# Kernel optimization log

Measured on AMD Instinct MI355X. Metric: run time of the kernel, lower is better.

The kernel has to match this reference:

```python
import jax, jax.numpy as jnp
import numpy as np

B, T = 64, 128
IN, H, L, OUT = 512, 1024, 2, 1


def _gru_scan(seq, Wi, Wh, bi, bh):
    # seq: (S, in_dim); PyTorch GRU cell, gate order r, z, n.
    h0 = jnp.zeros((H,), dtype=seq.dtype)
    def step(h, x):
        gi = x @ Wi.T + bi          # (3H,)
        gh = h @ Wh.T + bh          # (3H,)
        r = jax.nn.sigmoid(gi[:H] + gh[:H])
        z = jax.nn.sigmoid(gi[H:2 * H] + gh[H:2 * H])
        n = jnp.tanh(gi[2 * H:] + r * gh[2 * H:])
        h_new = (1.0 - z) * n + z * h
        return h_new, h_new
    _, hs = jax.lax.scan(step, h0, seq)
    return hs                        # (S, H)


def setup_inputs() -> dict:
    key = jax.random.key(0)
    ks = jax.random.split(key, 24)
    mk = lambda k, shape: jax.random.normal(k, shape, dtype=jnp.float32) * 0.05
    d = {}
    d['x'] = jax.random.normal(ks[0], (B, T, IN), dtype=jnp.float32)
    # gru1: layer0 input=IN, layer1 input=H
    d['g1_Wi0'] = mk(ks[1], (3 * H, IN)); d['g1_Wh0'] = mk(ks[2], (3 * H, H))
    d['g1_bi0'] = mk(ks[3], (3 * H,));    d['g1_bh0'] = mk(ks[4], (3 * H,))
    d['g1_Wi1'] = mk(ks[5], (3 * H, H));  d['g1_Wh1'] = mk(ks[6], (3 * H, H))
    d['g1_bi1'] = mk(ks[7], (3 * H,));    d['g1_bh1'] = mk(ks[8], (3 * H,))
    # gru2: both layers input=H
    d['g2_Wi0'] = mk(ks[9], (3 * H, H));  d['g2_Wh0'] = mk(ks[10], (3 * H, H))
    d['g2_bi0'] = mk(ks[11], (3 * H,));   d['g2_bh0'] = mk(ks[12], (3 * H,))
    d['g2_Wi1'] = mk(ks[13], (3 * H, H)); d['g2_Wh1'] = mk(ks[14], (3 * H, H))
    d['g2_bi1'] = mk(ks[15], (3 * H,));   d['g2_bh1'] = mk(ks[16], (3 * H,))
    d['fc1_W'] = mk(ks[17], (64, H));     d['fc1_b'] = mk(ks[18], (64,))
    d['fc2_W'] = mk(ks[19], (OUT, 64));   d['fc2_b'] = mk(ks[20], (OUT,))
    return d


def reference(x, g1_Wi0, g1_Wh0, g1_bi0, g1_bh0, g1_Wi1, g1_Wh1, g1_bi1, g1_bh1,
              g2_Wi0, g2_Wh0, g2_bi0, g2_bh0, g2_Wi1, g2_Wh1, g2_bi1, g2_bh1,
              fc1_W, fc1_b, fc2_W, fc2_b):
    # PyTorch feeds x[:, t, :] (2-D) to a batch_first GRU -> treated as an
    # UNBATCHED sequence of length B; hidden is carried across t. That equals
    # one GRU scan over the flattened (T*B)-step sequence, t-major / b-minor.
    seq = jnp.swapaxes(x, 0, 1).reshape(T * B, IN)
    hs0 = _gru_scan(seq, g1_Wi0, g1_Wh0, g1_bi0, g1_bh0)    # (T*B, H) layer 0
    hs1 = _gru_scan(hs0, g1_Wi1, g1_Wh1, g1_bi1, g1_bh1)    # (T*B, H) layer 1
    # h returned after timestep t is the hidden at flat step t*B + (B-1)
    s = jnp.stack([hs0, hs1], axis=1)[B - 1::B]             # (T, L, H)
    seq2 = s.reshape(T * L, H)                              # torch.cat(s)
    # gru2 over the [1, T*L, H] sequence (batch=1)
    hs2_0 = _gru_scan(seq2, g2_Wi0, g2_Wh0, g2_bi0, g2_bh0)
    hs2_1 = _gru_scan(hs2_0, g2_Wi1, g2_Wh1, g2_bi1, g2_bh1)
    h2 = jnp.stack([hs2_0[-1], hs2_1[-1]], axis=0)[:, None, :]  # (L, 1, H)
    y = jax.nn.sigmoid(h2 @ fc1_W.T + fc1_b)                # (L, 1, 64)
    out = jax.nn.sigmoid(y @ fc2_W.T + fc2_b)               # (L, 1, OUT)
    return out
```

## Files before the change

kernel.cpp:

```cpp
#include <hip/hip_runtime.h>


typedef unsigned u32x4 __attribute__((ext_vector_type(4)));
typedef _Float16 h2_t  __attribute__((ext_vector_type(2)));

#define S1 8192
#define S2 256

__device__ u32x4 g_h0s[S1][256];
__device__ u32x4 g_h1s[S1][256];
__device__ u32x4 g_q0s[S2][256];
__device__ u32x4 g_q1s[S2][256];
__device__ int   g_claim[128];

__device__ __forceinline__ unsigned pk(float a, float b) {
  unsigned short ua = __builtin_bit_cast(unsigned short, (_Float16)a);
  unsigned short ub = __builtin_bit_cast(unsigned short, (_Float16)b);
  return (unsigned)ua | ((unsigned)ub << 16);
}
__device__ __forceinline__ float unpk(unsigned u, int hi) {
  unsigned short us = (unsigned short)(hi ? (u >> 16) : (u & 0xffffu));
  return (float)__builtin_bit_cast(_Float16, us);
}

#if __has_builtin(__builtin_amdgcn_fdot2)
__device__ __forceinline__ float fdot2(unsigned a, unsigned b, float c) {
  return __builtin_amdgcn_fdot2(__builtin_bit_cast(h2_t, a),
                                __builtin_bit_cast(h2_t, b), c, false);
}
#else
__device__ __forceinline__ float fdot2(unsigned a, unsigned b, float c) {
  h2_t ha = __builtin_bit_cast(h2_t, a), hb = __builtin_bit_cast(h2_t, b);
  return c + (float)ha[0] * (float)hb[0] + (float)ha[1] * (float)hb[1];
}
#endif

__device__ __forceinline__ u32x4 ld_sc_v4(const u32x4* p) {
  u32x4 v;
  asm volatile("global_load_dwordx4 %0, %1, off sc1\n\t"
               "s_waitcnt vmcnt(0)" : "=&v"(v) : "v"(p) : "memory");
  return v;
}
__device__ __forceinline__ u32x4 ld_l2_v4(const u32x4* p) {
  u32x4 v;
  asm volatile("global_load_dwordx4 %0, %1, off sc0\n\t"
               "s_waitcnt vmcnt(0)" : "=&v"(v) : "v"(p) : "memory");
  return v;
}
__device__ __forceinline__ void st_sc_v4(u32x4* p, u32x4 v) {
  asm volatile("global_store_dwordx4 %0, %1, off sc1" :: "v"(p), "v"(v) : "memory");
}

__device__ __forceinline__ float rcpf(float x) {
#if __has_builtin(__builtin_amdgcn_rcpf)
  return __builtin_amdgcn_rcpf(x);
#else
  return 1.f / x;
#endif
}
__device__ __forceinline__ float sigf(float x) { return rcpf(1.f + __expf(-x)); }
__device__ __forceinline__ float tanh_f(float x) {
  x = fminf(fmaxf(x, -15.f), 15.f);
  const float e = __expf(2.f * x);
  return (e - 1.f) * rcpf(e + 1.f);
}

__device__ __forceinline__ int swzHc(int ch) { return ch ^ ((ch >> 3) & 7); }
__device__ __forceinline__ int swzH_pos(int i) { return (swzHc(i >> 2) << 2) | (i & 3); }
__device__ __forceinline__ int swzXc(int ch) { return ch ^ ((ch >> 2) & 7); }
__device__ __forceinline__ int swzX_pos(int i) { return (swzXc(i >> 2) << 2) | (i & 3); }

__global__ void init_all() {
  const long long NH = (long long)S1 * 256;
  const long long NQ = (long long)S2 * 256;
  const long long N  = 2 * NH + 2 * NQ;
  for (long long k = (long long)blockIdx.x * blockDim.x + threadIdx.x; k < N;
       k += (long long)gridDim.x * blockDim.x) {
    u32x4* r;
    long long k2 = k;
    if (k2 < NH) r = &g_h0s[0][0] + k2;
    else {
      k2 -= NH;
      if (k2 < NH) r = &g_h1s[0][0] + k2;
      else {
        k2 -= NH;
        if (k2 < NQ) r = &g_q0s[0][0] + k2;
        else         r = &g_q1s[0][0] + (k2 - NQ);
      }
    }
    (*r)[2] = 0xFFFFFFFFu;
  }
  if (blockIdx.x == 0 && threadIdx.x < 128) g_claim[threadIdx.x] = 0;
}

__device__ __forceinline__ const u32x4* in_addr(int role, int u, int r) {
  if (role == 1) return &g_h0s[u][r];
  if (role == 2) {
    const int ss = ((u >> 1) << 6) + 63;
    return (u & 1) ? &g_h1s[ss][r] : &g_h0s[ss][r];
  }
  return &g_q0s[u][r];
}
__device__ __forceinline__ unsigned in_want(int role, int u) {
  return (role == 2) ? (unsigned)(((u >> 1) << 6) + 63) : (unsigned)u;
}

#define MAC4(A, W4, H4)                                                       \
  A = fdot2((W4)[0], (H4)[0], A); A = fdot2((W4)[1], (H4)[1], A);             \
  A = fdot2((W4)[2], (H4)[2], A); A = fdot2((W4)[3], (H4)[3], A);

#define RED16(A)                                                              \
  A += __shfl_xor(A, 8, 16); A += __shfl_xor(A, 4, 16);                       \
  A += __shfl_xor(A, 2, 16); A += __shfl_xor(A, 1, 16);

__global__
__attribute__((amdgpu_flat_work_group_size(512, 512), amdgpu_waves_per_eu(2, 2)))
void gru_all(const float* __restrict__ x,
             const float* __restrict__ g1_Wi0, const float* __restrict__ g1_Wh0,
             const float* __restrict__ g1_bi0, const float* __restrict__ g1_bh0,
             const float* __restrict__ g1_Wi1, const float* __restrict__ g1_Wh1,
             const float* __restrict__ g1_bi1, const float* __restrict__ g1_bh1,
             const float* __restrict__ g2_Wi0, const float* __restrict__ g2_Wh0,
             const float* __restrict__ g2_bi0, const float* __restrict__ g2_bh0,
             const float* __restrict__ g2_Wi1, const float* __restrict__ g2_Wh1,
             const float* __restrict__ g2_bi1, const float* __restrict__ g2_bh1,
             const float* __restrict__ fc1W, const float* __restrict__ fc1b,
             const float* __restrict__ fc2W, const float* __restrict__ fc2b,
             float* __restrict__ out)
{
  const int tid = threadIdx.x;
  const int G   = tid >> 4;
  const int q   = tid & 15;
  const int rid = tid - 256;

  __shared__ __attribute__((aligned(16))) unsigned sH[2][512];
  __shared__ __attribute__((aligned(16))) unsigned sIN[8][512];
  __shared__ __attribute__((aligned(16))) unsigned sX[8][256];
  __shared__ float sD[96];
  __shared__ float sDI[96];
  __shared__ float sY[128];
  __shared__ int   sSlot;

  unsigned xcc;
  asm volatile("s_getreg_b32 %0, hwreg(HW_REG_XCC_ID)" : "=s"(xcc));
  xcc &= 7u;
  if (tid == 0) {
    int slot = -1;
    if (xcc < 4u) {
      for (int i = 0; i < 32 && slot < 0; ++i)
        if (atomicCAS(&g_claim[(int)xcc * 32 + i], 0, 1) == 0)
          slot = (int)xcc * 32 + i;
    }
    if (slot < 0) {
      for (int k = 0; k < 32; ++k) __builtin_amdgcn_s_sleep(64);
      for (int i = 0; i < 128 && slot < 0; ++i)
        if (atomicCAS(&g_claim[i], 0, 1) == 0) slot = i;
    }
    sSlot = slot;
  }
  __syncthreads();
  const int slot = sSlot;
  if (slot < 0) return;
  const int role = slot >> 5;
  const int rank = slot & 31;
  const int e0   = rank * 32;
  const bool lp  = ((int)xcc == role);
  const int S    = (role <= 1) ? S1 : S2;

  const float* Wh  = (role == 0) ? g1_Wh0 : (role == 1) ? g1_Wh1
                   : (role == 2) ? g2_Wh0 : g2_Wh1;
  const float* Wi  = (role == 0) ? g1_Wi0 : (role == 1) ? g1_Wi1
                   : (role == 2) ? g2_Wi0 : g2_Wi1;
  const float* pbi = (role == 0) ? g1_bi0 : (role == 1) ? g1_bi1
                   : (role == 2) ? g2_bi0 : g2_bi1;
  const float* pbh = (role == 0) ? g1_bh0 : (role == 1) ? g1_bh1
                   : (role == 2) ? g2_bh0 : g2_bh1;
  u32x4 (*outA)[256] = (role == 0) ? g_h0s : (role == 1) ? g_h1s
                     : (role == 2) ? g_q0s : g_q1s;

  u32x4 wv[6][8];
  {
    const bool isWh = (G < 16);
    const int  Gm   = isWh ? G : (G - 16);
    const float* M  = isWh ? Wh : Wi;
    const bool wide = isWh || (role != 0);
    #pragma unroll
    for (int j = 0; j < 6; ++j) {
      const int rr = Gm * 6 + j;
      const int R  = (rr >> 5) * 1024 + e0 + (rr & 31);
      if (wide) {
        const float4* rp = (const float4*)(M + (size_t)R * 1024 + 64 * q);
        #pragma unroll
        for (int c = 0; c < 8; ++c) {
          float4 a = rp[2 * c], b = rp[2 * c + 1];
          wv[j][c] = (u32x4){pk(a.x, a.y), pk(a.z, a.w), pk(b.x, b.y), pk(b.z, b.w)};
        }
      } else {
        const float4* rp = (const float4*)(M + (size_t)R * 512 + 32 * q);
        #pragma unroll
        for (int c = 0; c < 4; ++c) {
          float4 a = rp[2 * c], b = rp[2 * c + 1];
          wv[j][c] = (u32x4){pk(a.x, a.y), pk(a.z, a.w), pk(b.x, b.y), pk(b.z, b.w)};
        }
      }
    }
  }

  float bIr = 0, bIz = 0, bIn = 0, bHr = 0, bHz = 0, bHn = 0;
  if (tid < 32) {
    const int ge = e0 + tid;
    bIr = pbi[ge]; bIz = pbi[1024 + ge]; bIn = pbi[2048 + ge];
    bHr = pbh[ge]; bHz = pbh[1024 + ge]; bHn = pbh[2048 + ge];
  }

  if (tid >= 256) {
    if (role == 0) {
      #pragma unroll
      for (int u = 0; u < 4; ++u) {
        float2 xv = ((const float2*)(x + (size_t)((u & 63) * 128 + (u >> 6)) * 512))[rid];
        sX[u][swzX_pos(rid)] = pk(xv.x, xv.y);
      }
    } else {
      for (int u = 0; u < 4; ++u) {
        const u32x4* a = in_addr(role, u, rid);
        const unsigned w = in_want(role, u);
        u32x4 r = ld_sc_v4(a);
        while (r[2] != w) r = ld_sc_v4(a);
        sIN[u][swzH_pos(2 * rid)]     = r[0];
        sIN[u][swzH_pos(2 * rid + 1)] = r[1];
      }
    }
  }
  __syncthreads();

  for (int s = 0; s < S; ++s) {
    const int par = s & 1;

    if (tid >= 256 && (s & 3) == 0) {
      if (role == 0) {
        #pragma unroll
        for (int k = 0; k < 4; ++k) {
          const int u = s + 4 + k;
          if (u < S) {
            float2 xv = ((const float2*)(x + (size_t)((u & 63) * 128 + (u >> 6)) * 512))[rid];
            sX[u & 7][swzX_pos(rid)] = pk(xv.x, xv.y);
          }
        }
      } else {
        #pragma unroll
        for (int k = 0; k < 4; ++k) {
          const int u = s + 4 + k;
          if (u < S) {
            const u32x4* a = in_addr(role, u, rid);
            const unsigned w = in_want(role, u);
            u32x4 r = ld_sc_v4(a);
            while (r[2] != w) r = ld_sc_v4(a);
            sIN[u & 7][swzH_pos(2 * rid)]     = r[0];
            sIN[u & 7][swzH_pos(2 * rid + 1)] = r[1];
          }
        }
      }
    }

    if (tid < 256) {
      unsigned d0 = 0, d1 = 0;
      if (s > 0) {
        const unsigned w = (unsigned)(s - 1);
        const u32x4* a = &outA[s - 1][tid];
        u32x4 r;
        if (lp) {
          r = ld_l2_v4(a);
          int spin = 0;
          while (r[2] != w)
            r = (((++spin) & 7) == 0) ? ld_sc_v4(a) : ld_l2_v4(a);
        } else {
          r = ld_sc_v4(a);
          while (r[2] != w) r = ld_sc_v4(a);
        }
        d0 = r[0]; d1 = r[1];
      }
      sH[par][swzH_pos(2 * tid)]     = d0;
      sH[par][swzH_pos(2 * tid + 1)] = d1;
    }
    __syncthreads();

    float a0 = 0, a1 = 0, a2 = 0, a3 = 0, a4 = 0, a5 = 0;
    if (G < 16) {
      const u32x4* HV = (const u32x4*)sH[par];
      #pragma unroll
      for (int c = 0; c < 8; ++c) {
        const u32x4 h4 = HV[8 * q + (c ^ (q & 7))];
        MAC4(a0, wv[0][c], h4); MAC4(a1, wv[1][c], h4); MAC4(a2, wv[2][c], h4);
        MAC4(a3, wv[3][c], h4); MAC4(a4, wv[4][c], h4); MAC4(a5, wv[5][c], h4);
      }
    } else if (role != 0) {
      const u32x4* IV = (const u32x4*)sIN[s & 7];
      #pragma unroll
      for (int c = 0; c < 8; ++c) {
        const u32x4 h4 = IV[8 * q + (c ^ (q & 7))];
        MAC4(a0, wv[0][c], h4); MAC4(a1, wv[1][c], h4); MAC4(a2, wv[2][c], h4);
        MAC4(a3, wv[3][c], h4); MAC4(a4, wv[4][c], h4); MAC4(a5, wv[5][c], h4);
      }
    } else {
      const u32x4* XV = (const u32x4*)sX[s & 7];
      #pragma unroll
      for (int c = 0; c < 4; ++c) {
        const int ch = 4 * q + c;
        const u32x4 h4 = XV[ch ^ ((ch >> 2) & 7)];
        MAC4(a0, wv[0][c], h4); MAC4(a1, wv[1][c], h4); MAC4(a2, wv[2][c], h4);
        MAC4(a3, wv[3][c], h4); MAC4(a4, wv[4][c], h4); MAC4(a5, wv[5][c], h4);
      }
    }
    RED16(a0); RED16(a1); RED16(a2); RED16(a3); RED16(a4); RED16(a5);
    if (q < 6) {
      const float v = (q == 0) ? a0 : (q == 1) ? a1 : (q == 2) ? a2
                    : (q == 3) ? a3 : (q == 4) ? a4 : a5;
      if (G < 16) sD[G * 6 + q] = v;
      else        sDI[(G - 16) * 6 + q] = v;
    }
    __syncthreads();

    if (tid < 32) {
      const float rg = sigf(sDI[tid] + bIr + sD[tid] + bHr);
      const float zg = sigf(sDI[32 + tid] + bIz + sD[32 + tid] + bHz);
      const float ng = tanh_f(sDI[64 + tid] + bIn + rg * (sD[64 + tid] + bHn));
      const int ge = e0 + tid;
      const float hp = unpk(sH[par][swzH_pos(ge >> 1)], ge & 1);
      const float hn = (1.f - zg) * ng + zg * hp;
      const int b4 = (tid & 7) * 4;
      const float v0 = __shfl(hn, b4),     v1 = __shfl(hn, b4 + 1);
      const float v2 = __shfl(hn, b4 + 2), v3 = __shfl(hn, b4 + 3);
      if (tid < 8) {
        u32x4 rec = {pk(v0, v1), pk(v2, v3), (unsigned)s, 0u};
        st_sc_v4(&outA[s][rank * 8 + tid], rec);
      }
    }
  }

  if (role == 3 && rank == 0) {
    if (tid < 256) {
      const u32x4* a = &g_q0s[S2 - 1][tid];
      u32x4 r = ld_sc_v4(a);
      while (r[2] != (unsigned)(S2 - 1)) r = ld_sc_v4(a);
      sH[0][swzH_pos(2 * tid)]     = r[0];
      sH[0][swzH_pos(2 * tid + 1)] = r[1];
    } else {
      const u32x4* a = &g_q1s[S2 - 1][rid];
      u32x4 r = ld_sc_v4(a);
      while (r[2] != (unsigned)(S2 - 1)) r = ld_sc_v4(a);
      sH[1][swzH_pos(2 * rid)]     = r[0];
      sH[1][swzH_pos(2 * rid + 1)] = r[1];
    }
    __syncthreads();
    if (tid < 128) {
      const int l = tid >> 6, k = tid & 63;
      const unsigned* Hs = (const unsigned*)sH[l];
      const float* wrow = fc1W + (size_t)k * 1024;
      float acc = fc1b[k];
      for (int j2 = 0; j2 < 512; ++j2) {
        const unsigned hu = Hs[swzH_pos(j2)];
        acc += unpk(hu, 0) * wrow[2 * j2] + unpk(hu, 1) * wrow[2 * j2 + 1];
      }
      sY[tid] = sigf(acc);
    }
    __syncthreads();
    if (tid < 2) {
      const float* yv = sY + tid * 64;
      float acc = fc2b[0];
      for (int k2 = 0; k2 < 64; ++k2) acc += fc2W[k2] * yv[k2];
      out[tid] = sigf(acc);
    }
  }
}

extern "C" void kernel_launch(void* const* d_in, const int* in_sizes, int n_in,
                              void* d_out, int out_size, void* d_ws, size_t ws_size,
                              hipStream_t stream) {
  (void)in_sizes; (void)n_in; (void)out_size; (void)d_ws; (void)ws_size;
  const float* x      = (const float*)d_in[0];
  const float* g1_Wi0 = (const float*)d_in[1];
  const float* g1_Wh0 = (const float*)d_in[2];
  const float* g1_bi0 = (const float*)d_in[3];
  const float* g1_bh0 = (const float*)d_in[4];
  const float* g1_Wi1 = (const float*)d_in[5];
  const float* g1_Wh1 = (const float*)d_in[6];
  const float* g1_bi1 = (const float*)d_in[7];
  const float* g1_bh1 = (const float*)d_in[8];
  const float* g2_Wi0 = (const float*)d_in[9];
  const float* g2_Wh0 = (const float*)d_in[10];
  const float* g2_bi0 = (const float*)d_in[11];
  const float* g2_bh0 = (const float*)d_in[12];
  const float* g2_Wi1 = (const float*)d_in[13];
  const float* g2_Wh1 = (const float*)d_in[14];
  const float* g2_bi1 = (const float*)d_in[15];
  const float* g2_bh1 = (const float*)d_in[16];
  const float* fc1W   = (const float*)d_in[17];
  const float* fc1b   = (const float*)d_in[18];
  const float* fc2W   = (const float*)d_in[19];
  const float* fc2b   = (const float*)d_in[20];
  float* out = (float*)d_out;

  init_all<<<dim3(2048), dim3(256), 0, stream>>>();
  gru_all<<<dim3(256), dim3(512), 0, stream>>>(
      x, g1_Wi0, g1_Wh0, g1_bi0, g1_bh0, g1_Wi1, g1_Wh1, g1_bi1, g1_bh1,
      g2_Wi0, g2_Wh0, g2_bi0, g2_bh0, g2_Wi1, g2_Wh1, g2_bi1, g2_bh1,
      fc1W, fc1b, fc2W, fc2b, out);
}
```

Baseline: 25.51 ms.

## Exchange recurrent hidden state through double-buffered atomic 64-bit flag slots

Each block now publishes its newly computed hidden-state pairs into a small double-buffered array of 64-bit words, with the step number in the high half and packed fp16 data in the low half, using atomic exchange. Consumers poll these words with atomic reads, replacing the spin on the large per-step history buffer that used sc1 and L2 loads. The aim is to cut cross-XCD latency on the serial step-to-step dependency by using device-coherent atomics on a small hot region. In exchange, every step adds extra atomic traffic, and correctness now relies on the two-slot buffer never being overwritten before all readers have consumed it.

Result: no change. 25.44 ms (-0.3%).

```diff
diff --git a/kernel.cpp b/kernel.cpp
--- a/kernel.cpp
+++ b/kernel.cpp
@@ -11,6 +11,7 @@
 __device__ u32x4 g_h1s[S1][256];
 __device__ u32x4 g_q0s[S2][256];
 __device__ u32x4 g_q1s[S2][256];
+__device__ unsigned long long g_fast[4][2][512];
 __device__ int   g_claim[128];
 
 __device__ __forceinline__ unsigned pk(float a, float b) {
@@ -38,12 +39,6 @@
 __device__ __forceinline__ u32x4 ld_sc_v4(const u32x4* p) {
   u32x4 v;
   asm volatile("global_load_dwordx4 %0, %1, off sc1\n\t"
-               "s_waitcnt vmcnt(0)" : "=&v"(v) : "v"(p) : "memory");
-  return v;
-}
-__device__ __forceinline__ u32x4 ld_l2_v4(const u32x4* p) {
-  u32x4 v;
-  asm volatile("global_load_dwordx4 %0, %1, off sc0\n\t"
                "s_waitcnt vmcnt(0)" : "=&v"(v) : "v"(p) : "memory");
   return v;
 }
@@ -67,15 +62,18 @@
 
 __device__ __forceinline__ int swzHc(int ch) { return ch ^ ((ch >> 3) & 7); }
 __device__ __forceinline__ int swzH_pos(int i) { return (swzHc(i >> 2) << 2) | (i & 3); }
-__device__ __forceinline__ int swzXc(int ch) { return ch ^ ((ch >> 2) & 7); }
-__device__ __forceinline__ int swzX_pos(int i) { return (swzXc(i >> 2) << 2) | (i & 3); }
+__device__ __forceinline__ int swzX_pos(int i) {
+  int ch = i >> 2; ch ^= (ch >> 2) & 7; return (ch << 2) | (i & 3);
+}
 
 __global__ void init_all() {
   const long long NH = (long long)S1 * 256;
   const long long NQ = (long long)S2 * 256;
   const long long N  = 2 * NH + 2 * NQ;
-  for (long long k = (long long)blockIdx.x * blockDim.x + threadIdx.x; k < N;
-       k += (long long)gridDim.x * blockDim.x) {
+  u32x4 ff = {0u, 0u, 0xFFFFFFFFu, 0u};
+  const long long idx = (long long)blockIdx.x * blockDim.x + threadIdx.x;
+  const long long str = (long long)gridDim.x * blockDim.x;
+  for (long long k = idx; k < N; k += str) {
     u32x4* r;
     long long k2 = k;
     if (k2 < NH) r = &g_h0s[0][0] + k2;
@@ -88,8 +86,10 @@
         else         r = &g_q1s[0][0] + (k2 - NQ);
       }
     }
-    (*r)[2] = 0xFFFFFFFFu;
-  }
+    *r = ff;
+  }
+  for (long long k = idx; k < 4LL * 2 * 512; k += str)
+    ((unsigned long long*)g_fast)[k] = 0xFFFFFFFF00000000ULL;
   if (blockIdx.x == 0 && threadIdx.x < 128) g_claim[threadIdx.x] = 0;
 }
 
@@ -164,7 +164,6 @@
   const int role = slot >> 5;
   const int rank = slot & 31;
   const int e0   = rank * 32;
-  const bool lp  = ((int)xcc == role);
   const int S    = (role <= 1) ? S1 : S2;
 
   const float* Wh  = (role == 0) ? g1_Wh0 : (role == 1) ? g1_Wh1
@@ -266,18 +265,17 @@
       unsigned d0 = 0, d1 = 0;
       if (s > 0) {
         const unsigned w = (unsigned)(s - 1);
-        const u32x4* a = &outA[s - 1][tid];
-        u32x4 r;
-        if (lp) {
-          r = ld_l2_v4(a);
-          int spin = 0;
-          while (r[2] != w)
-            r = (((++spin) & 7) == 0) ? ld_sc_v4(a) : ld_l2_v4(a);
-        } else {
-          r = ld_sc_v4(a);
-          while (r[2] != w) r = ld_sc_v4(a);
+        unsigned long long* f0 = &g_fast[role][(s - 1) & 1][2 * tid];
+        unsigned long long* f1 = f0 + 1;
+        unsigned long long v0 = atomicAdd(f0, 0ull);
+        unsigned long long v1 = atomicAdd(f1, 0ull);
+        bool o0 = ((unsigned)(v0 >> 32) == w), o1 = ((unsigned)(v1 >> 32) == w);
+        while (!(o0 && o1)) {
+          if (!o0) v0 = atomicAdd(f0, 0ull);
+          if (!o1) v1 = atomicAdd(f1, 0ull);
+          o0 = ((unsigned)(v0 >> 32) == w); o1 = ((unsigned)(v1 >> 32) == w);
         }
-        d0 = r[0]; d1 = r[1];
+        d0 = (unsigned)v0; d1 = (unsigned)v1;
       }
       sH[par][swzH_pos(2 * tid)]     = d0;
       sH[par][swzH_pos(2 * tid + 1)] = d1;
@@ -327,9 +325,16 @@
       const int ge = e0 + tid;
       const float hp = unpk(sH[par][swzH_pos(ge >> 1)], ge & 1);
       const float hn = (1.f - zg) * ng + zg * hp;
+      const int i2 = (tid & 15) * 2;
+      const float p0 = __shfl(hn, i2), p1 = __shfl(hn, i2 + 1);
       const int b4 = (tid & 7) * 4;
       const float v0 = __shfl(hn, b4),     v1 = __shfl(hn, b4 + 1);
       const float v2 = __shfl(hn, b4 + 2), v3 = __shfl(hn, b4 + 3);
+      if (tid < 16) {
+        unsigned long long val =
+            ((unsigned long long)(unsigned)s << 32) | (unsigned long long)pk(p0, p1);
+        atomicExch(&g_fast[role][s & 1][rank * 16 + tid], val);
+      }
       if (tid < 8) {
         u32x4 rec = {pk(v0, v1), pk(v2, v3), (unsigned)s, 0u};
         st_sc_v4(&outA[s][rank * 8 + tid], rec);
```
